# Performance work log

Measured on AMD Instinct MI355X. Metric: run time of the kernel, lower is better.

## Reference

```python
import jax, jax.numpy as jnp
import numpy as np
import math

EMBED_DIM = 512
NUM_HEADS = 8
NUM_LAYERS = 6
NUM_CLASSES = 8
MAX_POS = 100
LN_EPS = 1e-5


def setup_inputs() -> dict:
    key = jax.random.key(0)
    ks = jax.random.split(key, 12)
    D, H, L, C = EMBED_DIM, NUM_HEADS, NUM_LAYERS, NUM_CLASSES
    B, M = 64, 20
    s = 0.02
    def p(k, shape):
        return jax.random.normal(k, shape, jnp.float32) * s
    return {
        "context_tokens": jax.random.normal(ks[0], (B, M, D), jnp.float32),
        "pos_enc": jax.random.normal(ks[1], (1, MAX_POS, D), jnp.float32),
        "sa_w": p(ks[2], (L, 3 * D, D)), "sa_b": jnp.zeros((L, 3 * D), jnp.float32),
        "sa_ow": p(ks[3], (L, D, D)), "sa_ob": jnp.zeros((L, D), jnp.float32),
        "ca_w": p(ks[4], (L, 3 * D, D)), "ca_b": jnp.zeros((L, 3 * D), jnp.float32),
        "ca_ow": p(ks[5], (L, D, D)), "ca_ob": jnp.zeros((L, D), jnp.float32),
        "ln1_g": jnp.ones((L, D), jnp.float32), "ln1_b": jnp.zeros((L, D), jnp.float32),
        "ln2_g": jnp.ones((L, D), jnp.float32), "ln2_b": jnp.zeros((L, D), jnp.float32),
        "ln3_g": jnp.ones((L, D), jnp.float32), "ln3_b": jnp.zeros((L, D), jnp.float32),
        "ffn_w1": p(ks[6], (L, 4 * D, D)), "ffn_b1": jnp.zeros((L, 4 * D), jnp.float32),
        "ffn_w2": p(ks[7], (L, D, 4 * D)), "ffn_b2": jnp.zeros((L, D), jnp.float32),
        "out_w": p(ks[8], (C, D)), "out_b": jnp.zeros((C,), jnp.float32),
        "max_tokens": 30,
    }


def _ln(x, g, b):
    m = jnp.mean(x, axis=-1, keepdims=True)
    v = jnp.mean(jnp.square(x - m), axis=-1, keepdims=True)
    return (x - m) * jax.lax.rsqrt(v + LN_EPS) * g + b


def _mha(q_in, kv_in, w, b, ow, ob, causal):
    # w: (3D, D) packed q/k/v projections (PyTorch in_proj), ow: (D, D)
    D = q_in.shape[-1]
    H = NUM_HEADS
    hd = D // H
    qw, kw, vw = w[:D], w[D:2 * D], w[2 * D:]
    bq, bk, bv = b[:D], b[D:2 * D], b[2 * D:]
    q = q_in @ qw.T + bq
    k = kv_in @ kw.T + bk
    v = kv_in @ vw.T + bv
    B, Sq = q.shape[0], q.shape[1]
    Sk = k.shape[1]
    q = q.reshape(B, Sq, H, hd)
    k = k.reshape(B, Sk, H, hd)
    v = v.reshape(B, Sk, H, hd)
    scores = jnp.einsum('bqhd,bkhd->bhqk', q, k) * (1.0 / math.sqrt(hd))
    if causal:
        mask = jnp.tril(jnp.ones((Sq, Sk), dtype=bool))
        scores = jnp.where(mask, scores, -jnp.inf)
    attn = jax.nn.softmax(scores, axis=-1)
    out = jnp.einsum('bhqk,bkhd->bqhd', attn, v).reshape(B, Sq, D)
    return out @ ow.T + ob


def _forward(context_tokens, pos_enc, sa_w, sa_b, sa_ow, sa_ob, ca_w, ca_b,
             ca_ow, ca_ob, ln1_g, ln1_b, ln2_g, ln2_b, ln3_g, ln3_b,
             ffn_w1, ffn_b1, ffn_w2, ffn_b2, out_w, out_b, max_tokens):
    gen = context_tokens  # (B, M, D), grows each step (full recompute, no KV cache)
    outs = []
    for t in range(max_tokens):
        S = gen.shape[1]
        x = gen + pos_enc[:, :S, :]
        for i in range(NUM_LAYERS):
            # norm_first pre-LN GPT-2 style TransformerDecoderLayer
            x = x + _mha(_ln(x, ln1_g[i], ln1_b[i]), _ln(x, ln1_g[i], ln1_b[i]),
                         sa_w[i], sa_b[i], sa_ow[i], sa_ob[i], causal=True)
            x = x + _mha(_ln(x, ln2_g[i], ln2_b[i]), context_tokens,
                         ca_w[i], ca_b[i], ca_ow[i], ca_ob[i], causal=False)
            h = _ln(x, ln3_g[i], ln3_b[i])
            h = jax.nn.gelu(h @ ffn_w1[i].T + ffn_b1[i], approximate=False)
            x = x + (h @ ffn_w2[i].T + ffn_b2[i])
        last = x[:, -1:, :]
        outs.append(last @ out_w.T + out_b)
        gen = jnp.concatenate([gen, last], axis=1)
    return jnp.concatenate(outs, axis=1)  # (B, max_tokens, num_classes)


def reference(context_tokens, pos_enc, sa_w, sa_b, sa_ow, sa_ob, ca_w, ca_b,
              ca_ow, ca_ob, ln1_g, ln1_b, ln2_g, ln2_b, ln3_g, ln3_b,
              ffn_w1, ffn_b1, ffn_w2, ffn_b2, out_w, out_b, max_tokens):
    return _forward(context_tokens, pos_enc, sa_w, sa_b, sa_ow, sa_ob, ca_w, ca_b,
                    ca_ow, ca_ob, ln1_g, ln1_b, ln2_g, ln2_b, ln3_g, ln3_b,
                    ffn_w1, ffn_b1, ffn_w2, ffn_b2, out_w, out_b, max_tokens)
```

## Files before the change

kernel.cpp:

```cpp
#include <hip/hip_runtime.h>
#include <math.h>

#define F4(p) (*reinterpret_cast<const float4*>(p))

constexpr int D    = 512;
constexpr int H    = 8;
constexpr int HD   = 64;
constexpr int NL   = 6;
constexpr int NB   = 64;
constexpr int M    = 20;
constexpr int T    = 30;
constexpr int SMAX = 49;
constexpr int NR   = NB * M;
constexpr float EPS   = 1e-5f;
constexpr float SCALE = 0.125f;

#define GM_PLAIN 0
#define GM_QKV   1

__device__ __forceinline__ float wave_sum(float v){
  #pragma unroll
  for (int o = 32; o > 0; o >>= 1) v += __shfl_down(v, o, 64);
  return v;
}

__device__ __forceinline__ float block_sum(float v, float* red){
  v = wave_sum(v);
  int wid = threadIdx.x >> 6, lane = threadIdx.x & 63;
  if (lane == 0) red[wid] = v;
  __syncthreads();
  if (threadIdx.x == 0) red[0] = red[0] + red[1] + red[2] + red[3];
  __syncthreads();
  float tot = red[0];
  __syncthreads();
  return tot;
}

__device__ __forceinline__ float gelu_f(float x){
  return 0.5f * x * (1.f + erff(x * 0.70710678118654752f));
}

template<int K>
__device__ __forceinline__ float dot8(const float* __restrict__ w, const float* x, int j){
  float a0 = 0.f, a1 = 0.f;
  #pragma unroll
  for (int r = 0; r < K/64; r++){
    int d = j*4 + r*64;
    float4 w0 = F4(w + d);        float4 w1 = F4(w + d + 32);
    float4 x0 = F4(x + d);        float4 x1 = F4(x + d + 32);
    a0 += w0.x*x0.x + w0.y*x0.y + w0.z*x0.z + w0.w*x0.w;
    a1 += w1.x*x1.x + w1.y*x1.y + w1.z*x1.z + w1.w*x1.w;
  }
  float a = a0 + a1;
  a += __shfl_xor(a, 4, 8);
  a += __shfl_xor(a, 2, 8);
  a += __shfl_xor(a, 1, 8);
  return a;
}


__global__ __launch_bounds__(256) void k_embed(const float* __restrict__ ctx,
    const float* __restrict__ pos, float* __restrict__ X0){
  int r = blockIdx.x, t = threadIdx.x, s = r % M;
  X0[(size_t)r*D + t]       = ctx[(size_t)r*D + t]       + pos[(size_t)s*D + t];
  X0[(size_t)r*D + t + 256] = ctx[(size_t)r*D + t + 256] + pos[(size_t)s*D + t + 256];
}

__global__ __launch_bounds__(256) void k_ln(const float* __restrict__ x, float* __restrict__ y,
    const float* __restrict__ g, const float* __restrict__ bb){
  __shared__ float red[4];
  int r = blockIdx.x, t = threadIdx.x;
  const float* xr = x + (size_t)r*D;
  float v0 = xr[t], v1 = xr[t+256];
  float mean = block_sum(v0+v1, red) * (1.f/D);
  float d0 = v0-mean, d1 = v1-mean;
  float var = block_sum(d0*d0 + d1*d1, red) * (1.f/D);
  float rs = rsqrtf(var + EPS);
  float* yr = y + (size_t)r*D;
  yr[t]     = d0*rs*g[t]     + bb[t];
  yr[t+256] = d1*rs*g[t+256] + bb[t+256];
}

__global__ __launch_bounds__(256) void k_gemm(
    const float* __restrict__ A, const float* __restrict__ W,
    const float* __restrict__ bias, const float* __restrict__ res,
    float* __restrict__ C, int K, int ldc, int gelu_flag,
    float* __restrict__ q0, float* __restrict__ kc, float* __restrict__ vc, int mode){
  __shared__ __align__(16) float As[32][64];
  __shared__ __align__(16) float Ws[32][64];
  int m0 = blockIdx.x*64, n0 = blockIdx.y*64;
  int t = threadIdx.x, tx = t & 15, ty = t >> 4;
  float acc[4][4] = {};
  for (int k0 = 0; k0 < K; k0 += 32){
    #pragma unroll
    for (int i = 0; i < 2; i++){
      int idx = t + i*256;
      int m = idx & 63, k4 = idx >> 6;
      float4 a = F4(A + (size_t)(m0+m)*K + k0 + k4*4);
      As[k4*4+0][m]=a.x; As[k4*4+1][m]=a.y; As[k4*4+2][m]=a.z; As[k4*4+3][m]=a.w;
      float4 w = F4(W + (size_t)(n0+m)*K + k0 + k4*4);
      Ws[k4*4+0][m]=w.x; Ws[k4*4+1][m]=w.y; Ws[k4*4+2][m]=w.z; Ws[k4*4+3][m]=w.w;
    }
    __syncthreads();
    #pragma unroll
    for (int k = 0; k < 32; k++){
      float4 a = *reinterpret_cast<float4*>(&As[k][ty*4]);
      float4 w = *reinterpret_cast<float4*>(&Ws[k][tx*4]);
      float av[4] = {a.x,a.y,a.z,a.w};
      float wv[4] = {w.x,w.y,w.z,w.w};
      #pragma unroll
      for (int i = 0; i < 4; i++)
        #pragma unroll
        for (int jj = 0; jj < 4; jj++) acc[i][jj] += av[i]*wv[jj];
    }
    __syncthreads();
  }
  #pragma unroll
  for (int i = 0; i < 4; i++){
    int row = m0 + ty*4 + i;
    #pragma unroll
    for (int jj = 0; jj < 4; jj++){
      int col = n0 + tx*4 + jj;
      float v = acc[i][jj] + bias[col];
      if (res) v += res[(size_t)row*ldc + col];
      if (gelu_flag) v = gelu_f(v);
      if (mode == GM_PLAIN){
        C[(size_t)row*ldc + col] = v;
      } else {
        if (col < D) q0[(size_t)row*D + col] = v;
        else {
          int b = row / M, s = row % M;
          float* dst = (col < 2*D) ? kc : vc;
          dst[((size_t)b*SMAX + s)*D + (col & (D-1))] = v;
        }
      }
    }
  }
}

__global__ __launch_bounds__(256) void k_sattn_pre(const float* __restrict__ Q0,
    const float* __restrict__ kc, const float* __restrict__ vc, float* __restrict__ AT0){
  int b = blockIdx.x >> 3, h = blockIdx.x & 7, t = threadIdx.x;
  __shared__ __align__(16) float q[M][HD], kk[M][HD], vv[M][HD];
  __shared__ float sc[M][M];
  for (int idx = t; idx < M*HD; idx += 256){
    int s = idx >> 6, e = idx & 63;
    q[s][e]  = Q0[((size_t)b*M + s)*D + h*HD + e];
    kk[s][e] = kc[((size_t)b*SMAX + s)*D + h*HD + e];
    vv[s][e] = vc[((size_t)b*SMAX + s)*D + h*HD + e];
  }
  __syncthreads();
  for (int idx = t; idx < M*M; idx += 256){
    int qs = idx / M, ks = idx % M;
    if (ks <= qs){
      float s = 0.f;
      #pragma unroll
      for (int e = 0; e < HD; e++) s += q[qs][e]*kk[ks][e];
      sc[qs][ks] = s * SCALE;
    }
  }
  __syncthreads();
  if (t < M){
    float mx = -1e30f;
    for (int ks = 0; ks <= t; ks++) mx = fmaxf(mx, sc[t][ks]);
    float sum = 0.f;
    for (int ks = 0; ks <= t; ks++){ float e = expf(sc[t][ks]-mx); sc[t][ks] = e; sum += e; }
    float inv = 1.f/sum;
    for (int ks = 0; ks <= t; ks++) sc[t][ks] *= inv;
  }
  __syncthreads();
  for (int idx = t; idx < M*HD; idx += 256){
    int qs = idx >> 6, e = idx & 63;
    float o = 0.f;
    for (int ks = 0; ks <= qs; ks++) o += sc[qs][ks]*vv[ks][e];
    AT0[((size_t)b*M + qs)*D + h*HD + e] = o;
  }
}

__global__ __launch_bounds__(256) void k_cattn_pre(const float* __restrict__ Q0,
    const float* __restrict__ ckv, float* __restrict__ AT0){
  int b = blockIdx.x >> 3, h = blockIdx.x & 7, t = threadIdx.x;
  __shared__ __align__(16) float q[M][HD], kk[M][HD], vv[M][HD];
  __shared__ float sc[M][M];
  for (int idx = t; idx < M*HD; idx += 256){
    int s = idx >> 6, e = idx & 63;
    q[s][e]  = Q0[((size_t)b*M + s)*D + h*HD + e];
    kk[s][e] = ckv[((size_t)b*M + s)*1024 + h*HD + e];
    vv[s][e] = ckv[((size_t)b*M + s)*1024 + D + h*HD + e];
  }
  __syncthreads();
  for (int idx = t; idx < M*M; idx += 256){
    int qs = idx / M, ks = idx % M;
    float s = 0.f;
    #pragma unroll
    for (int e = 0; e < HD; e++) s += q[qs][e]*kk[ks][e];
    sc[qs][ks] = s * SCALE;
  }
  __syncthreads();
  if (t < M){
    float mx = -1e30f;
    for (int ks = 0; ks < M; ks++) mx = fmaxf(mx, sc[t][ks]);
    float sum = 0.f;
    for (int ks = 0; ks < M; ks++){ float e = expf(sc[t][ks]-mx); sc[t][ks] = e; sum += e; }
    float inv = 1.f/sum;
    for (int ks = 0; ks < M; ks++) sc[t][ks] *= inv;
  }
  __syncthreads();
  for (int idx = t; idx < M*HD; idx += 256){
    int qs = idx >> 6, e = idx & 63;
    float o = 0.f;
    for (int ks = 0; ks < M; ks++) o += sc[qs][ks]*vv[ks][e];
    AT0[((size_t)b*M + qs)*D + h*HD + e] = o;
  }
}

__global__ __launch_bounds__(256) void k_copy_last(const float* __restrict__ X0,
    float* __restrict__ xb){
  int b = blockIdx.x, t = threadIdx.x;
  xb[(size_t)b*D + t]       = X0[((size_t)b*M + M-1)*D + t];
  xb[(size_t)b*D + t + 256] = X0[((size_t)b*M + M-1)*D + t + 256];
}

__global__ __launch_bounds__(256) void k_final(float* __restrict__ xb,
    const float* __restrict__ pos, const float* __restrict__ ow, const float* __restrict__ ob,
    float* __restrict__ out, int tstep, int pnext){
  int b = blockIdx.x, t = threadIdx.x;
  __shared__ __align__(16) float x[D];
  x[t] = xb[(size_t)b*D + t]; x[t+256] = xb[(size_t)b*D + t + 256];
  __syncthreads();
  int c = t >> 5, lane = t & 31;
  float a = 0.f;
  for (int d = lane*4; d < D; d += 128){
    float4 wv = F4(ow + (size_t)c*D + d);
    a += wv.x*x[d] + wv.y*x[d+1] + wv.z*x[d+2] + wv.w*x[d+3];
  }
  a += __shfl_xor(a, 16, 32); a += __shfl_xor(a, 8, 32);
  a += __shfl_xor(a, 4, 32);  a += __shfl_xor(a, 2, 32); a += __shfl_xor(a, 1, 32);
  if (lane == 0) out[((size_t)b*T + tstep)*8 + c] = a + ob[c];
  xb[(size_t)b*D + t]       = x[t]     + pos[(size_t)pnext*D + t];
  xb[(size_t)b*D + t + 256] = x[t+256] + pos[(size_t)pnext*D + t + 256];
}


__global__ __launch_bounds__(256) void k_dqkv(const float* __restrict__ xb,
    const float* __restrict__ w, const float* __restrict__ bias,
    const float* __restrict__ g, const float* __restrict__ bb,
    float* __restrict__ qb, float* __restrict__ kc, float* __restrict__ vc, int p){
  __shared__ __align__(16) float xn[D];
  __shared__ float red[4];
  int blk = blockIdx.x, b = blk/6, ch = blk%6, t = threadIdx.x, j = t & 7;
  float v0 = xb[(size_t)b*D + t], v1 = xb[(size_t)b*D + t + 256];
  float mean = block_sum(v0+v1, red) * (1.f/D);
  float d0 = v0-mean, d1 = v1-mean;
  float var = block_sum(d0*d0 + d1*d1, red) * (1.f/D);
  float rs = rsqrtf(var + EPS);
  xn[t]     = d0*rs*g[t]     + bb[t];
  xn[t+256] = d1*rs*g[t+256] + bb[t+256];
  __syncthreads();
  #pragma unroll
  for (int pass = 0; pass < 8; pass++){
    int o = ch*256 + pass*32 + (t >> 3);
    float r = dot8<512>(w + (size_t)o*D, xn, j);
    if (j == 0){
      r += bias[o];
      if (o < D)        qb[(size_t)b*D + o] = r;
      else if (o < 2*D) kc[((size_t)b*SMAX + p)*D + o - D]   = r;
      else              vc[((size_t)b*SMAX + p)*D + o - 2*D] = r;
    }
  }
}

__global__ __launch_bounds__(256) void k_dmid(float* __restrict__ xb,
    const float* __restrict__ qb,
    const float* __restrict__ kc, const float* __restrict__ vc, const float* __restrict__ ckv,
    const float* __restrict__ sow, const float* __restrict__ sob,
    const float* __restrict__ cqw, const float* __restrict__ cqb,
    const float* __restrict__ cow, const float* __restrict__ cob,
    const float* __restrict__ g2, const float* __restrict__ b2,
    const float* __restrict__ g3, const float* __restrict__ b3,
    float* __restrict__ xnb, int p){
  int b = blockIdx.x, t = threadIdx.x, j = t & 7, S = p + 1;
  __shared__ __align__(16) float q[D], at[D], x1[D], xn[D];
  __shared__ float sc[H][SMAX+3];
  __shared__ float red[4];
  q[t] = qb[(size_t)b*D + t]; q[t+256] = qb[(size_t)b*D + t + 256];
  __syncthreads();
  const float* kb = kc + (size_t)b*SMAX*D;
  const float* vb = vc + (size_t)b*SMAX*D;
  for (int idx = t; idx < H*S; idx += 256){
    int h = idx / S, ks = idx % S;
    const float* kr = kb + (size_t)ks*D + h*HD;
    float s = 0.f;
    #pragma unroll
    for (int e = 0; e < HD; e += 4){
      float4 kv = F4(kr + e);
      s += kv.x*q[h*HD+e] + kv.y*q[h*HD+e+1] + kv.z*q[h*HD+e+2] + kv.w*q[h*HD+e+3];
    }
    sc[h][ks] = s * SCALE;
  }
  __syncthreads();
  if (t < H){
    float mx = -1e30f;
    for (int ks = 0; ks < S; ks++) mx = fmaxf(mx, sc[t][ks]);
    float sum = 0.f;
    for (int ks = 0; ks < S; ks++){ float e = expf(sc[t][ks]-mx); sc[t][ks] = e; sum += e; }
    float inv = 1.f/sum;
    for (int ks = 0; ks < S; ks++) sc[t][ks] *= inv;
  }
  __syncthreads();
  for (int idx = t; idx < D; idx += 256){
    int h = idx >> 6, e = idx & 63;
    float o = 0.f;
    for (int ks = 0; ks < S; ks++) o += sc[h][ks]*vb[(size_t)ks*D + h*HD + e];
    at[idx] = o;
  }
  __syncthreads();
  #pragma unroll
  for (int pass = 0; pass < 16; pass++){
    int o = pass*32 + (t >> 3);
    float r = dot8<512>(sow + (size_t)o*D, at, j);
    if (j == 0) x1[o] = r + sob[o] + xb[(size_t)b*D + o];
  }
  __syncthreads();
  {
    float v0 = x1[t], v1 = x1[t+256];
    float mean = block_sum(v0+v1, red) * (1.f/D);
    float d0 = v0-mean, d1 = v1-mean;
    float var = block_sum(d0*d0 + d1*d1, red) * (1.f/D);
    float rs = rsqrtf(var + EPS);
    xn[t]     = d0*rs*g2[t]     + b2[t];
    xn[t+256] = d1*rs*g2[t+256] + b2[t+256];
  }
  __syncthreads();
  #pragma unroll
  for (int pass = 0; pass < 16; pass++){
    int o = pass*32 + (t >> 3);
    float r = dot8<512>(cqw + (size_t)o*D, xn, j);
    if (j == 0) q[o] = r + cqb[o];
  }
  __syncthreads();
  const float* cb_ = ckv + (size_t)b*M*1024;
  for (int idx = t; idx < H*M; idx += 256){
    int h = idx / M, ks = idx % M;
    const float* kr = cb_ + (size_t)ks*1024 + h*HD;
    float s = 0.f;
    #pragma unroll
    for (int e = 0; e < HD; e += 4){
      float4 kv = F4(kr + e);
      s += kv.x*q[h*HD+e] + kv.y*q[h*HD+e+1] + kv.z*q[h*HD+e+2] + kv.w*q[h*HD+e+3];
    }
    sc[h][ks] = s * SCALE;
  }
  __syncthreads();
  if (t < H){
    float mx = -1e30f;
    for (int ks = 0; ks < M; ks++) mx = fmaxf(mx, sc[t][ks]);
    float sum = 0.f;
    for (int ks = 0; ks < M; ks++){ float e = expf(sc[t][ks]-mx); sc[t][ks] = e; sum += e; }
    float inv = 1.f/sum;
    for (int ks = 0; ks < M; ks++) sc[t][ks] *= inv;
  }
  __syncthreads();
  for (int idx = t; idx < D; idx += 256){
    int h = idx >> 6, e = idx & 63;
    float o = 0.f;
    for (int ks = 0; ks < M; ks++) o += sc[h][ks]*cb_[(size_t)ks*1024 + D + h*HD + e];
    at[idx] = o;
  }
  __syncthreads();
  #pragma unroll
  for (int pass = 0; pass < 16; pass++){
    int o = pass*32 + (t >> 3);
    float r = dot8<512>(cow + (size_t)o*D, at, j);
    if (j == 0){ float nx = x1[o] + r + cob[o]; x1[o] = nx; xb[(size_t)b*D + o] = nx; }
  }
  __syncthreads();
  {
    float v0 = x1[t], v1 = x1[t+256];
    float mean = block_sum(v0+v1, red) * (1.f/D);
    float d0 = v0-mean, d1 = v1-mean;
    float var = block_sum(d0*d0 + d1*d1, red) * (1.f/D);
    float rs = rsqrtf(var + EPS);
    xnb[(size_t)b*D + t]       = d0*rs*g3[t]     + b3[t];
    xnb[(size_t)b*D + t + 256] = d1*rs*g3[t+256] + b3[t+256];
  }
}

__global__ __launch_bounds__(256) void k_dffn1(const float* __restrict__ xnb,
    const float* __restrict__ w1, const float* __restrict__ b1, float* __restrict__ hb){
  int blk = blockIdx.x, b = blk >> 3, ch = blk & 7, t = threadIdx.x, j = t & 7;
  __shared__ __align__(16) float xn[D];
  xn[t] = xnb[(size_t)b*D + t]; xn[t+256] = xnb[(size_t)b*D + t + 256];
  __syncthreads();
  #pragma unroll
  for (int pass = 0; pass < 8; pass++){
    int o = ch*256 + pass*32 + (t >> 3);
    float r = dot8<512>(w1 + (size_t)o*D, xn, j);
    if (j == 0) hb[(size_t)b*2048 + o] = gelu_f(r + b1[o]);
  }
}

__global__ __launch_bounds__(256) void k_dffn2(const float* __restrict__ hb,
    const float* __restrict__ w2, const float* __restrict__ b2, float* __restrict__ xb){
  int blk = blockIdx.x, b = blk >> 1, hf = blk & 1, t = threadIdx.x, j = t & 7;
  __shared__ __align__(16) float hh[2048];
  #pragma unroll
  for (int i = 0; i < 8; i++) hh[t + i*256] = hb[(size_t)b*2048 + t + i*256];
  __syncthreads();
  #pragma unroll
  for (int pass = 0; pass < 8; pass++){
    int o = hf*256 + pass*32 + (t >> 3);
    float r = dot8<2048>(w2 + (size_t)o*2048, hh, j);
    if (j == 0) xb[(size_t)b*D + o] += r + b2[o];
  }
}


extern "C" void kernel_launch(void* const* d_in, const int* in_sizes, int n_in,
                              void* d_out, int out_size, void* d_ws, size_t ws_size,
                              hipStream_t stream){
  (void)in_sizes; (void)n_in; (void)out_size; (void)ws_size;
  const float* ctx   = (const float*)d_in[0];
  const float* pos   = (const float*)d_in[1];
  const float* sa_w  = (const float*)d_in[2];
  const float* sa_b  = (const float*)d_in[3];
  const float* sa_ow = (const float*)d_in[4];
  const float* sa_ob = (const float*)d_in[5];
  const float* ca_w  = (const float*)d_in[6];
  const float* ca_b  = (const float*)d_in[7];
  const float* ca_ow = (const float*)d_in[8];
  const float* ca_ob = (const float*)d_in[9];
  const float* ln1g  = (const float*)d_in[10];
  const float* ln1b  = (const float*)d_in[11];
  const float* ln2g  = (const float*)d_in[12];
  const float* ln2b  = (const float*)d_in[13];
  const float* ln3g  = (const float*)d_in[14];
  const float* ln3b  = (const float*)d_in[15];
  const float* fw1   = (const float*)d_in[16];
  const float* fb1   = (const float*)d_in[17];
  const float* fw2   = (const float*)d_in[18];
  const float* fb2   = (const float*)d_in[19];
  const float* outw  = (const float*)d_in[20];
  const float* outb  = (const float*)d_in[21];
  float* out = (float*)d_out;

  float* w = (float*)d_ws;
  size_t off = 0;
  auto alloc = [&](size_t n){ float* p = w + off; off += n; return p; };
  float* kcache = alloc((size_t)NL*NB*SMAX*D);
  float* vcache = alloc((size_t)NL*NB*SMAX*D);
  float* ckv    = alloc((size_t)NL*NB*M*1024);
  float* X0     = alloc((size_t)NR*D);
  float* XN0    = alloc((size_t)NR*D);
  float* Q0     = alloc((size_t)NR*D);
  float* AT0    = alloc((size_t)NR*D);
  float* H0     = alloc((size_t)NR*2048);
  float* xb     = alloc((size_t)NB*D);
  float* qb     = alloc((size_t)NB*D);
  float* xnb    = alloc((size_t)NB*D);
  float* hb     = alloc((size_t)NB*2048);

  dim3 blk(256);

  k_embed<<<NR, blk, 0, stream>>>(ctx, pos, X0);
  for (int l = 0; l < NL; l++){
    k_gemm<<<dim3(NR/64, 1024/64), blk, 0, stream>>>(
        ctx, ca_w + (size_t)l*3*D*D + (size_t)D*D, ca_b + (size_t)l*3*D + D, nullptr,
        ckv + (size_t)l*NB*M*1024, 512, 1024, 0, nullptr, nullptr, nullptr, GM_PLAIN);
  }

  for (int l = 0; l < NL; l++){
    const float* saw = sa_w + (size_t)l*3*D*D;
    const float* sab = sa_b + (size_t)l*3*D;
    float* kcl = kcache + (size_t)l*NB*SMAX*D;
    float* vcl = vcache + (size_t)l*NB*SMAX*D;
    const float* ckl = ckv + (size_t)l*NB*M*1024;

    k_ln<<<NR, blk, 0, stream>>>(X0, XN0, ln1g + l*D, ln1b + l*D);
    k_gemm<<<dim3(NR/64, 1536/64), blk, 0, stream>>>(
        XN0, saw, sab, nullptr, nullptr, 512, D, 0, Q0, kcl, vcl, GM_QKV);
    k_sattn_pre<<<NB*H, blk, 0, stream>>>(Q0, kcl, vcl, AT0);
    k_gemm<<<dim3(NR/64, D/64), blk, 0, stream>>>(
        AT0, sa_ow + (size_t)l*D*D, sa_ob + l*D, X0, X0, 512, D, 0,
        nullptr, nullptr, nullptr, GM_PLAIN);
    k_ln<<<NR, blk, 0, stream>>>(X0, XN0, ln2g + l*D, ln2b + l*D);
    k_gemm<<<dim3(NR/64, D/64), blk, 0, stream>>>(
        XN0, ca_w + (size_t)l*3*D*D, ca_b + (size_t)l*3*D, nullptr, Q0, 512, D, 0,
        nullptr, nullptr, nullptr, GM_PLAIN);
    k_cattn_pre<<<NB*H, blk, 0, stream>>>(Q0, ckl, AT0);
    k_gemm<<<dim3(NR/64, D/64), blk, 0, stream>>>(
        AT0, ca_ow + (size_t)l*D*D, ca_ob + l*D, X0, X0, 512, D, 0,
        nullptr, nullptr, nullptr, GM_PLAIN);
    k_ln<<<NR, blk, 0, stream>>>(X0, XN0, ln3g + l*D, ln3b + l*D);
    k_gemm<<<dim3(NR/64, 2048/64), blk, 0, stream>>>(
        XN0, fw1 + (size_t)l*2048*D, fb1 + (size_t)l*2048, nullptr, H0, 512, 2048, 1,
        nullptr, nullptr, nullptr, GM_PLAIN);
    k_gemm<<<dim3(NR/64, D/64), blk, 0, stream>>>(
        H0, fw2 + (size_t)l*D*2048, fb2 + l*D, X0, X0, 2048, D, 0,
        nullptr, nullptr, nullptr, GM_PLAIN);
  }
  k_copy_last<<<NB, blk, 0, stream>>>(X0, xb);
  k_final<<<NB, blk, 0, stream>>>(xb, pos, outw, outb, out, 0, M);

  for (int t = 1; t < T; t++){
    int p = M - 1 + t;
    for (int l = 0; l < NL; l++){
      float* kcl = kcache + (size_t)l*NB*SMAX*D;
      float* vcl = vcache + (size_t)l*NB*SMAX*D;
      const float* ckl = ckv + (size_t)l*NB*M*1024;
      k_dqkv<<<NB*6, blk, 0, stream>>>(xb, sa_w + (size_t)l*3*D*D, sa_b + (size_t)l*3*D,
          ln1g + l*D, ln1b + l*D, qb, kcl, vcl, p);
      k_dmid<<<NB, blk, 0, stream>>>(xb, qb, kcl, vcl, ckl,
          sa_ow + (size_t)l*D*D, sa_ob + l*D,
          ca_w + (size_t)l*3*D*D, ca_b + (size_t)l*3*D,
          ca_ow + (size_t)l*D*D, ca_ob + l*D,
          ln2g + l*D, ln2b + l*D, ln3g + l*D, ln3b + l*D, xnb, p);
      k_dffn1<<<NB*8, blk, 0, stream>>>(xnb, fw1 + (size_t)l*2048*D, fb1 + (size_t)l*2048, hb);
      k_dffn2<<<NB*2, blk, 0, stream>>>(hb, fw2 + (size_t)l*D*2048, fb2 + l*D, xb);
    }
    k_final<<<NB, blk, 0, stream>>>(xb, pos, outw, outb, out, t, M + t);
  }
}
```

Before: 40.71 ms.

## Fuse entire autoregressive decode loop into one persistent per-batch kernel

Replaces the per-step, per-layer launches (qkv, mid, ffn1, ffn2, final) with a single 1024-thread kernel per batch element that runs all 29 decode steps and 6 layers internally. Activations stay in shared memory and synchronisation uses block barriers. This removes roughly 700 launches and the global round-trips of intermediate buffers. In exchange, only 64 blocks run, so each block streams all layer weights serially from L2/HBM with low occupancy, and FFN work is no longer spread across 8 or 2 blocks per batch element.

```diff
diff --git a/kernel.cpp b/kernel.cpp
--- a/kernel.cpp
+++ b/kernel.cpp
@@ -18,24 +18,6 @@
 #define GM_PLAIN 0
 #define GM_QKV   1
 
-__device__ __forceinline__ float wave_sum(float v){
-  #pragma unroll
-  for (int o = 32; o > 0; o >>= 1) v += __shfl_down(v, o, 64);
-  return v;
-}
-
-__device__ __forceinline__ float block_sum(float v, float* red){
-  v = wave_sum(v);
-  int wid = threadIdx.x >> 6, lane = threadIdx.x & 63;
-  if (lane == 0) red[wid] = v;
-  __syncthreads();
-  if (threadIdx.x == 0) red[0] = red[0] + red[1] + red[2] + red[3];
-  __syncthreads();
-  float tot = red[0];
-  __syncthreads();
-  return tot;
-}
-
 __device__ __forceinline__ float gelu_f(float x){
   return 0.5f * x * (1.f + erff(x * 0.70710678118654752f));
 }
@@ -58,6 +40,42 @@
   return a;
 }
 
+__device__ __forceinline__ float dot16_2048(const float* __restrict__ w, const float* x, int j){
+  float a0 = 0.f, a1 = 0.f;
+  #pragma unroll
+  for (int r = 0; r < 16; r++){
+    int d = j*4 + r*128;
+    float4 w0 = F4(w + d);        float4 w1 = F4(w + d + 64);
+    float4 x0 = F4(x + d);        float4 x1 = F4(x + d + 64);
+    a0 += w0.x*x0.x + w0.y*x0.y + w0.z*x0.z + w0.w*x0.w;
+    a1 += w1.x*x1.x + w1.y*x1.y + w1.z*x1.z + w1.w*x1.w;
+  }
+  float a = a0 + a1;
+  a += __shfl_xor(a, 8, 16);
+  a += __shfl_xor(a, 4, 16);
+  a += __shfl_xor(a, 2, 16);
+  a += __shfl_xor(a, 1, 16);
+  return a;
+}
+
+
+__device__ __forceinline__ float wave_sum64(float v){
+  #pragma unroll
+  for (int o = 32; o > 0; o >>= 1) v += __shfl_down(v, o, 64);
+  return v;
+}
+
+__device__ __forceinline__ float block_sum256(float v, float* red){
+  v = wave_sum64(v);
+  int wid = threadIdx.x >> 6, lane = threadIdx.x & 63;
+  if (lane == 0) red[wid] = v;
+  __syncthreads();
+  if (threadIdx.x == 0) red[0] = red[0] + red[1] + red[2] + red[3];
+  __syncthreads();
+  float tot = red[0];
+  __syncthreads();
+  return tot;
+}
 
 __global__ __launch_bounds__(256) void k_embed(const float* __restrict__ ctx,
     const float* __restrict__ pos, float* __restrict__ X0){
@@ -72,9 +90,9 @@
   int r = blockIdx.x, t = threadIdx.x;
   const float* xr = x + (size_t)r*D;
   float v0 = xr[t], v1 = xr[t+256];
-  float mean = block_sum(v0+v1, red) * (1.f/D);
+  float mean = block_sum256(v0+v1, red) * (1.f/D);
   float d0 = v0-mean, d1 = v1-mean;
-  float var = block_sum(d0*d0 + d1*d1, red) * (1.f/D);
+  float var = block_sum256(d0*d0 + d1*d1, red) * (1.f/D);
   float rs = rsqrtf(var + EPS);
   float* yr = y + (size_t)r*D;
   yr[t]     = d0*rs*g[t]     + bb[t];
@@ -214,204 +232,238 @@
   }
 }
 
-__global__ __launch_bounds__(256) void k_copy_last(const float* __restrict__ X0,
-    float* __restrict__ xb){
-  int b = blockIdx.x, t = threadIdx.x;
-  xb[(size_t)b*D + t]       = X0[((size_t)b*M + M-1)*D + t];
-  xb[(size_t)b*D + t + 256] = X0[((size_t)b*M + M-1)*D + t + 256];
-}
-
-__global__ __launch_bounds__(256) void k_final(float* __restrict__ xb,
-    const float* __restrict__ pos, const float* __restrict__ ow, const float* __restrict__ ob,
-    float* __restrict__ out, int tstep, int pnext){
-  int b = blockIdx.x, t = threadIdx.x;
-  __shared__ __align__(16) float x[D];
-  x[t] = xb[(size_t)b*D + t]; x[t+256] = xb[(size_t)b*D + t + 256];
-  __syncthreads();
-  int c = t >> 5, lane = t & 31;
-  float a = 0.f;
-  for (int d = lane*4; d < D; d += 128){
-    float4 wv = F4(ow + (size_t)c*D + d);
-    a += wv.x*x[d] + wv.y*x[d+1] + wv.z*x[d+2] + wv.w*x[d+3];
-  }
-  a += __shfl_xor(a, 16, 32); a += __shfl_xor(a, 8, 32);
-  a += __shfl_xor(a, 4, 32);  a += __shfl_xor(a, 2, 32); a += __shfl_xor(a, 1, 32);
-  if (lane == 0) out[((size_t)b*T + tstep)*8 + c] = a + ob[c];
-  xb[(size_t)b*D + t]       = x[t]     + pos[(size_t)pnext*D + t];
-  xb[(size_t)b*D + t + 256] = x[t+256] + pos[(size_t)pnext*D + t + 256];
-}
-
-
-__global__ __launch_bounds__(256) void k_dqkv(const float* __restrict__ xb,
-    const float* __restrict__ w, const float* __restrict__ bias,
-    const float* __restrict__ g, const float* __restrict__ bb,
-    float* __restrict__ qb, float* __restrict__ kc, float* __restrict__ vc, int p){
-  __shared__ __align__(16) float xn[D];
-  __shared__ float red[4];
-  int blk = blockIdx.x, b = blk/6, ch = blk%6, t = threadIdx.x, j = t & 7;
-  float v0 = xb[(size_t)b*D + t], v1 = xb[(size_t)b*D + t + 256];
-  float mean = block_sum(v0+v1, red) * (1.f/D);
-  float d0 = v0-mean, d1 = v1-mean;
-  float var = block_sum(d0*d0 + d1*d1, red) * (1.f/D);
-  float rs = rsqrtf(var + EPS);
-  xn[t]     = d0*rs*g[t]     + bb[t];
-  xn[t+256] = d1*rs*g[t+256] + bb[t+256];
-  __syncthreads();
+
+__device__ __forceinline__ float bsum1024(float v, float* red, int t){
   #pragma unroll
-  for (int pass = 0; pass < 8; pass++){
-    int o = ch*256 + pass*32 + (t >> 3);
-    float r = dot8<512>(w + (size_t)o*D, xn, j);
-    if (j == 0){
-      r += bias[o];
-      if (o < D)        qb[(size_t)b*D + o] = r;
-      else if (o < 2*D) kc[((size_t)b*SMAX + p)*D + o - D]   = r;
-      else              vc[((size_t)b*SMAX + p)*D + o - 2*D] = r;
-    }
-  }
-}
-
-__global__ __launch_bounds__(256) void k_dmid(float* __restrict__ xb,
-    const float* __restrict__ qb,
-    const float* __restrict__ kc, const float* __restrict__ vc, const float* __restrict__ ckv,
-    const float* __restrict__ sow, const float* __restrict__ sob,
-    const float* __restrict__ cqw, const float* __restrict__ cqb,
-    const float* __restrict__ cow, const float* __restrict__ cob,
-    const float* __restrict__ g2, const float* __restrict__ b2,
-    const float* __restrict__ g3, const float* __restrict__ b3,
-    float* __restrict__ xnb, int p){
-  int b = blockIdx.x, t = threadIdx.x, j = t & 7, S = p + 1;
-  __shared__ __align__(16) float q[D], at[D], x1[D], xn[D];
-  __shared__ float sc[H][SMAX+3];
-  __shared__ float red[4];
-  q[t] = qb[(size_t)b*D + t]; q[t+256] = qb[(size_t)b*D + t + 256];
-  __syncthreads();
-  const float* kb = kc + (size_t)b*SMAX*D;
-  const float* vb = vc + (size_t)b*SMAX*D;
-  for (int idx = t; idx < H*S; idx += 256){
-    int h = idx / S, ks = idx % S;
-    const float* kr = kb + (size_t)ks*D + h*HD;
+  for (int o = 32; o > 0; o >>= 1) v += __shfl_xor(v, o, 64);
+  if ((t & 63) == 0) red[t >> 6] = v;
+  __syncthreads();
+  if (t == 0){
     float s = 0.f;
     #pragma unroll
-    for (int e = 0; e < HD; e += 4){
-      float4 kv = F4(kr + e);
-      s += kv.x*q[h*HD+e] + kv.y*q[h*HD+e+1] + kv.z*q[h*HD+e+2] + kv.w*q[h*HD+e+3];
+    for (int i = 0; i < 16; i++) s += red[i];
+    red[16] = s;
+  }
+  __syncthreads();
+  return red[16];
+}
+
+__device__ __forceinline__ void ln_ip(const float* xx, float* yy,
+    const float* __restrict__ g, const float* __restrict__ bb, float* red, int t){
+  float v = (t < D) ? xx[t] : 0.f;
+  float mean = bsum1024(v, red, t) * (1.f/D);
+  float dd = (t < D) ? (v - mean) : 0.f;
+  float var = bsum1024(dd*dd, red, t) * (1.f/D);
+  float rs = rsqrtf(var + EPS);
+  if (t < D) yy[t] = dd*rs*g[t] + bb[t];
+}
+
+__device__ __forceinline__ void logits_pos(float* x, const float* __restrict__ outw,
+    const float* __restrict__ outb, const float* __restrict__ pos,
+    float* __restrict__ out, int b, int t, int st, int pn){
+  if (t < D){
+    int c = t >> 6, lane = t & 63;
+    const float* wr = outw + (size_t)c*D + lane*8;
+    const float* xr = x + lane*8;
+    float4 w0 = F4(wr), w1 = F4(wr + 4);
+    float4 x0 = F4(xr), x1 = F4(xr + 4);
+    float a = w0.x*x0.x + w0.y*x0.y + w0.z*x0.z + w0.w*x0.w
+            + w1.x*x1.x + w1.y*x1.y + w1.z*x1.z + w1.w*x1.w;
+    #pragma unroll
+    for (int o = 32; o > 0; o >>= 1) a += __shfl_xor(a, o, 64);
+    if (lane == 0) out[((size_t)b*T + st)*8 + c] = a + outb[c];
+  }
+  __syncthreads();
+  if (t < D) x[t] += pos[(size_t)pn*D + t];
+  __syncthreads();
+}
+
+__global__ __launch_bounds__(1024) void k_chain(
+    const float* __restrict__ X0, const float* __restrict__ pos,
+    const float* __restrict__ sa_w, const float* __restrict__ sa_b,
+    const float* __restrict__ sa_ow, const float* __restrict__ sa_ob,
+    const float* __restrict__ ca_w, const float* __restrict__ ca_b,
+    const float* __restrict__ ca_ow, const float* __restrict__ ca_ob,
+    const float* __restrict__ ln1g, const float* __restrict__ ln1b,
+    const float* __restrict__ ln2g, const float* __restrict__ ln2b,
+    const float* __restrict__ ln3g, const float* __restrict__ ln3b,
+    const float* __restrict__ fw1, const float* __restrict__ fb1,
+    const float* __restrict__ fw2, const float* __restrict__ fb2,
+    const float* __restrict__ outw, const float* __restrict__ outb,
+    float* __restrict__ kcache, float* __restrict__ vcache,
+    const float* __restrict__ ckv, float* __restrict__ out)
+{
+  const int b = blockIdx.x, t = threadIdx.x;
+  const int j8 = t & 7, j16 = t & 15;
+  __shared__ __align__(16) float x[D], xn[D], q[D], at[D], kcur[D], vcur[D];
+  __shared__ __align__(16) float hh[2048];
+  __shared__ float sc[H][SMAX + 7];
+  __shared__ float red[17];
+
+  if (t < D) x[t] = X0[((size_t)b*M + (M-1))*D + t];
+  __syncthreads();
+
+  logits_pos(x, outw, outb, pos, out, b, t, 0, M);
+
+  for (int st = 1; st < T; st++){
+    const int p = M - 1 + st, S = p + 1;
+    for (int l = 0; l < NL; l++){
+      float* kb = kcache + ((size_t)l*NB + b)*SMAX*D;
+      float* vb = vcache + ((size_t)l*NB + b)*SMAX*D;
+      const float* cb_ = ckv + ((size_t)l*NB + b)*M*1024;
+
+      ln_ip(x, xn, ln1g + l*D, ln1b + l*D, red, t);
+      __syncthreads();
+
+      {
+        const float* w = sa_w + (size_t)l*3*D*D;
+        const float* bias = sa_b + (size_t)l*3*D;
+        for (int pass = 0; pass < 12; pass++){
+          int o = pass*128 + (t >> 3);
+          float r = dot8<512>(w + (size_t)o*D, xn, j8);
+          if (j8 == 0){
+            r += bias[o];
+            if (o < D) q[o] = r;
+            else if (o < 2*D){ kcur[o-D] = r; kb[(size_t)p*D + (o-D)] = r; }
+            else { vcur[o-2*D] = r; vb[(size_t)p*D + (o-2*D)] = r; }
+          }
+        }
+      }
+      __syncthreads();
+
+      {
+        int h = t >> 7, kslot = (t & 127) >> 3;
+        const float* qh = q + h*HD;
+        float4 x0 = F4(qh + j8*4), x1 = F4(qh + j8*4 + 32);
+        for (int ks = kslot; ks < S; ks += 16){
+          const float* kr = (ks == p) ? (kcur + h*HD) : (kb + (size_t)ks*D + h*HD);
+          float4 w0 = F4(kr + j8*4), w1 = F4(kr + j8*4 + 32);
+          float a = w0.x*x0.x + w0.y*x0.y + w0.z*x0.z + w0.w*x0.w
+                  + w1.x*x1.x + w1.y*x1.y + w1.z*x1.z + w1.w*x1.w;
+          a += __shfl_xor(a, 4, 8); a += __shfl_xor(a, 2, 8); a += __shfl_xor(a, 1, 8);
+          if (j8 == 0) sc[h][ks] = a * SCALE;
+        }
+      }
+      __syncthreads();
+      if ((t >> 6) < H){
+        int h = t >> 6, lane = t & 63;
+        float v = (lane < S) ? sc[h][lane] : -1e30f;
+        float mx = v;
+        #pragma unroll
+        for (int o = 32; o > 0; o >>= 1) mx = fmaxf(mx, __shfl_xor(mx, o, 64));
+        float e = (lane < S) ? expf(v - mx) : 0.f;
+        float sum = e;
+        #pragma unroll
+        for (int o = 32; o > 0; o >>= 1) sum += __shfl_xor(sum, o, 64);
+        if (lane < S) sc[h][lane] = e / sum;
+      }
+      __syncthreads();
+      if (t < D){
+        int h = t >> 6, e = t & 63;
+        float o2 = 0.f;
+        for (int ks = 0; ks < p; ks++) o2 += sc[h][ks] * vb[(size_t)ks*D + h*HD + e];
+        o2 += sc[h][p] * vcur[h*HD + e];
+        at[t] = o2;
+      }
+      __syncthreads();
+
+      {
+        const float* w = sa_ow + (size_t)l*D*D;
+        const float* bias = sa_ob + (size_t)l*D;
+        for (int pass = 0; pass < 4; pass++){
+          int o = pass*128 + (t >> 3);
+          float r = dot8<512>(w + (size_t)o*D, at, j8);
+          if (j8 == 0) x[o] += r + bias[o];
+        }
+      }
+      __syncthreads();
+
+      ln_ip(x, xn, ln2g + l*D, ln2b + l*D, red, t);
+      __syncthreads();
+
+      {
+        const float* w = ca_w + (size_t)l*3*D*D;
+        const float* bias = ca_b + (size_t)l*3*D;
+        for (int pass = 0; pass < 4; pass++){
+          int o = pass*128 + (t >> 3);
+          float r = dot8<512>(w + (size_t)o*D, xn, j8);
+          if (j8 == 0) q[o] = r + bias[o];
+        }
+      }
+      __syncthreads();
+
+      {
+        int h = t >> 7, kslot = (t & 127) >> 3;
+        const float* qh = q + h*HD;
+        float4 x0 = F4(qh + j8*4), x1 = F4(qh + j8*4 + 32);
+        for (int ks = kslot; ks < M; ks += 16){
+          const float* kr = cb_ + (size_t)ks*1024 + h*HD;
+          float4 w0 = F4(kr + j8*4), w1 = F4(kr + j8*4 + 32);
+          float a = w0.x*x0.x + w0.y*x0.y + w0.z*x0.z + w0.w*x0.w
+                  + w1.x*x1.x + w1.y*x1.y + w1.z*x1.z + w1.w*x1.w;
+          a += __shfl_xor(a, 4, 8); a += __shfl_xor(a, 2, 8); a += __shfl_xor(a, 1, 8);
+          if (j8 == 0) sc[h][ks] = a * SCALE;
+        }
+      }
+      __syncthreads();
+      if ((t >> 6) < H){
+        int h = t >> 6, lane = t & 63;
+        float v = (lane < M) ? sc[h][lane] : -1e30f;
+        float mx = v;
+        #pragma unroll
+        for (int o = 32; o > 0; o >>= 1) mx = fmaxf(mx, __shfl_xor(mx, o, 64));
+        float e = (lane < M) ? expf(v - mx) : 0.f;
+        float sum = e;
+        #pragma unroll
+        for (int o = 32; o > 0; o >>= 1) sum += __shfl_xor(sum, o, 64);
+        if (lane < M) sc[h][lane] = e / sum;
+      }
+      __syncthreads();
+      if (t < D){
+        int h = t >> 6, e = t & 63;
+        float o2 = 0.f;
+        for (int ks = 0; ks < M; ks++) o2 += sc[h][ks] * cb_[(size_t)ks*1024 + D + h*HD + e];
+        at[t] = o2;
+      }
+      __syncthreads();
+
+      {
+        const float* w = ca_ow + (size_t)l*D*D;
+        const float* bias = ca_ob + (size_t)l*D;
+        for (int pass = 0; pass < 4; pass++){
+          int o = pass*128 + (t >> 3);
+          float r = dot8<512>(w + (size_t)o*D, at, j8);
+          if (j8 == 0) x[o] += r + bias[o];
+        }
+      }
+      __syncthreads();
+
+      ln_ip(x, xn, ln3g + l*D, ln3b + l*D, red, t);
+      __syncthreads();
+
+      {
+        const float* w = fw1 + (size_t)l*2048*D;
+        const float* bias = fb1 + (size_t)l*2048;
+        for (int pass = 0; pass < 16; pass++){
+          int o = pass*128 + (t >> 3);
+          float r = dot8<512>(w + (size_t)o*D, xn, j8);
+          if (j8 == 0) hh[o] = gelu_f(r + bias[o]);
+        }
+      }
+      __syncthreads();
+
+      {
+        const float* w = fw2 + (size_t)l*D*2048;
+        const float* bias = fb2 + (size_t)l*D;
+        for (int pass = 0; pass < 8; pass++){
+          int o = pass*64 + (t >> 4);
+          float r = dot16_2048(w + (size_t)o*2048, hh, j16);
+          if (j16 == 0) x[o] += r + bias[o];
+        }
+      }
+      __syncthreads();
     }
-    sc[h][ks] = s * SCALE;
-  }
-  __syncthreads();
-  if (t < H){
-    float mx = -1e30f;
-    for (int ks = 0; ks < S; ks++) mx = fmaxf(mx, sc[t][ks]);
-    float sum = 0.f;
-    for (int ks = 0; ks < S; ks++){ float e = expf(sc[t][ks]-mx); sc[t][ks] = e; sum += e; }
-    float inv = 1.f/sum;
-    for (int ks = 0; ks < S; ks++) sc[t][ks] *= inv;
-  }
-  __syncthreads();
-  for (int idx = t; idx < D; idx += 256){
-    int h = idx >> 6, e = idx & 63;
-    float o = 0.f;
-    for (int ks = 0; ks < S; ks++) o += sc[h][ks]*vb[(size_t)ks*D + h*HD + e];
-    at[idx] = o;
-  }
-  __syncthreads();
-  #pragma unroll
-  for (int pass = 0; pass < 16; pass++){
-    int o = pass*32 + (t >> 3);
-    float r = dot8<512>(sow + (size_t)o*D, at, j);
-    if (j == 0) x1[o] = r + sob[o] + xb[(size_t)b*D + o];
-  }
-  __syncthreads();
-  {
-    float v0 = x1[t], v1 = x1[t+256];
-    float mean = block_sum(v0+v1, red) * (1.f/D);
-    float d0 = v0-mean, d1 = v1-mean;
-    float var = block_sum(d0*d0 + d1*d1, red) * (1.f/D);
-    float rs = rsqrtf(var + EPS);
-    xn[t]     = d0*rs*g2[t]     + b2[t];
-    xn[t+256] = d1*rs*g2[t+256] + b2[t+256];
-  }
-  __syncthreads();
-  #pragma unroll
-  for (int pass = 0; pass < 16; pass++){
-    int o = pass*32 + (t >> 3);
-    float r = dot8<512>(cqw + (size_t)o*D, xn, j);
-    if (j == 0) q[o] = r + cqb[o];
-  }
-  __syncthreads();
-  const float* cb_ = ckv + (size_t)b*M*1024;
-  for (int idx = t; idx < H*M; idx += 256){
-    int h = idx / M, ks = idx % M;
-    const float* kr = cb_ + (size_t)ks*1024 + h*HD;
-    float s = 0.f;
-    #pragma unroll
-    for (int e = 0; e < HD; e += 4){
-      float4 kv = F4(kr + e);
-      s += kv.x*q[h*HD+e] + kv.y*q[h*HD+e+1] + kv.z*q[h*HD+e+2] + kv.w*q[h*HD+e+3];
-    }
-    sc[h][ks] = s * SCALE;
-  }
-  __syncthreads();
-  if (t < H){
-    float mx = -1e30f;
-    for (int ks = 0; ks < M; ks++) mx = fmaxf(mx, sc[t][ks]);
-    float sum = 0.f;
-    for (int ks = 0; ks < M; ks++){ float e = expf(sc[t][ks]-mx); sc[t][ks] = e; sum += e; }
-    float inv = 1.f/sum;
-    for (int ks = 0; ks < M; ks++) sc[t][ks] *= inv;
-  }
-  __syncthreads();
-  for (int idx = t; idx < D; idx += 256){
-    int h = idx >> 6, e = idx & 63;
-    float o = 0.f;
-    for (int ks = 0; ks < M; ks++) o += sc[h][ks]*cb_[(size_t)ks*1024 + D + h*HD + e];
-    at[idx] = o;
-  }
-  __syncthreads();
-  #pragma unroll
-  for (int pass = 0; pass < 16; pass++){
-    int o = pass*32 + (t >> 3);
-    float r = dot8<512>(cow + (size_t)o*D, at, j);
-    if (j == 0){ float nx = x1[o] + r + cob[o]; x1[o] = nx; xb[(size_t)b*D + o] = nx; }
-  }
-  __syncthreads();
-  {
-    float v0 = x1[t], v1 = x1[t+256];
-    float mean = block_sum(v0+v1, red) * (1.f/D);
-    float d0 = v0-mean, d1 = v1-mean;
-    float var = block_sum(d0*d0 + d1*d1, red) * (1.f/D);
-    float rs = rsqrtf(var + EPS);
-    xnb[(size_t)b*D + t]       = d0*rs*g3[t]     + b3[t];
-    xnb[(size_t)b*D + t + 256] = d1*rs*g3[t+256] + b3[t+256];
-  }
-}
-
-__global__ __launch_bounds__(256) void k_dffn1(const float* __restrict__ xnb,
-    const float* __restrict__ w1, const float* __restrict__ b1, float* __restrict__ hb){
-  int blk = blockIdx.x, b = blk >> 3, ch = blk & 7, t = threadIdx.x, j = t & 7;
-  __shared__ __align__(16) float xn[D];
-  xn[t] = xnb[(size_t)b*D + t]; xn[t+256] = xnb[(size_t)b*D + t + 256];
-  __syncthreads();
-  #pragma unroll
-  for (int pass = 0; pass < 8; pass++){
-    int o = ch*256 + pass*32 + (t >> 3);
-    float r = dot8<512>(w1 + (size_t)o*D, xn, j);
-    if (j == 0) hb[(size_t)b*2048 + o] = gelu_f(r + b1[o]);
-  }
-}
-
-__global__ __launch_bounds__(256) void k_dffn2(const float* __restrict__ hb,
-    const float* __restrict__ w2, const float* __restrict__ b2, float* __restrict__ xb){
-  int blk = blockIdx.x, b = blk >> 1, hf = blk & 1, t = threadIdx.x, j = t & 7;
-  __shared__ __align__(16) float hh[2048];
-  #pragma unroll
-  for (int i = 0; i < 8; i++) hh[t + i*256] = hb[(size_t)b*2048 + t + i*256];
-  __syncthreads();
-  #pragma unroll
-  for (int pass = 0; pass < 8; pass++){
-    int o = hf*256 + pass*32 + (t >> 3);
-    float r = dot8<2048>(w2 + (size_t)o*2048, hh, j);
-    if (j == 0) xb[(size_t)b*D + o] += r + b2[o];
+    logits_pos(x, outw, outb, pos, out, b, t, st, M + st);
   }
 }
 
@@ -455,10 +507,6 @@
   float* Q0     = alloc((size_t)NR*D);
   float* AT0    = alloc((size_t)NR*D);
   float* H0     = alloc((size_t)NR*2048);
-  float* xb     = alloc((size_t)NB*D);
-  float* qb     = alloc((size_t)NB*D);
-  float* xnb    = alloc((size_t)NB*D);
-  float* hb     = alloc((size_t)NB*2048);
 
   dim3 blk(256);
 
@@ -499,25 +547,9 @@
         H0, fw2 + (size_t)l*D*2048, fb2 + l*D, X0, X0, 2048, D, 0,
         nullptr, nullptr, nullptr, GM_PLAIN);
   }
-  k_copy_last<<<NB, blk, 0, stream>>>(X0, xb);
-  k_final<<<NB, blk, 0, stream>>>(xb, pos, outw, outb, out, 0, M);
-
-  for (int t = 1; t < T; t++){
-    int p = M - 1 + t;
-    for (int l = 0; l < NL; l++){
-      float* kcl = kcache + (size_t)l*NB*SMAX*D;
-      float* vcl = vcache + (size_t)l*NB*SMAX*D;
-      const float* ckl = ckv + (size_t)l*NB*M*1024;
-      k_dqkv<<<NB*6, blk, 0, stream>>>(xb, sa_w + (size_t)l*3*D*D, sa_b + (size_t)l*3*D,
-          ln1g + l*D, ln1b + l*D, qb, kcl, vcl, p);
-      k_dmid<<<NB, blk, 0, stream>>>(xb, qb, kcl, vcl, ckl,
-          sa_ow + (size_t)l*D*D, sa_ob + l*D,
-          ca_w + (size_t)l*3*D*D, ca_b + (size_t)l*3*D,
-          ca_ow + (size_t)l*D*D, ca_ob + l*D,
-          ln2g + l*D, ln2b + l*D, ln3g + l*D, ln3b + l*D, xnb, p);
-      k_dffn1<<<NB*8, blk, 0, stream>>>(xnb, fw1 + (size_t)l*2048*D, fb1 + (size_t)l*2048, hb);
-      k_dffn2<<<NB*2, blk, 0, stream>>>(hb, fw2 + (size_t)l*D*2048, fb2 + l*D, xb);
-    }
-    k_final<<<NB, blk, 0, stream>>>(xb, pos, outw, outb, out, t, M + t);
-  }
-}
+
+  k_chain<<<NB, dim3(1024), 0, stream>>>(
+      X0, pos, sa_w, sa_b, sa_ow, sa_ob, ca_w, ca_b, ca_ow, ca_ob,
+      ln1g, ln1b, ln2g, ln2b, ln3g, ln3b, fw1, fb1, fw2, fb2,
+      outw, outb, kcache, vcache, ckv, out);
+}
```

New measurement: 42.30 ms. 1.04x slower.
